# Optimization experiments

Hardware: AMD Instinct MI355X
Metric: run time of the kernel (lower is better)

## Reference

```python
import jax, jax.numpy as jnp
import numpy as np

N, E = 50000, 800000
D, H = 256, 256
OA, OS, OE = 21, 2, 5


def _sage(x, src, dst, wl, bl, wr):
    # PyG SAGEConv: out = lin_l(mean_{j in N(i)} x_j) + lin_r(x_i); bias lives in lin_l
    n = x.shape[0]
    msg = x[src]                                            # [E, d] gather
    agg = jax.ops.segment_sum(msg, dst, num_segments=n)     # [N, d]
    cnt = jax.ops.segment_sum(jnp.ones((src.shape[0],), x.dtype), dst, num_segments=n)
    mean = agg / jnp.maximum(cnt, 1.0)[:, None]
    return mean @ wl.T + bl + x @ wr.T


def _bn(x, g, b, eps=1e-5):
    mu = x.mean(axis=0)
    var = x.var(axis=0)
    return (x - mu) * jax.lax.rsqrt(var + eps) * g + b


def setup_inputs() -> dict:
    key = jax.random.key(0)
    ks = jax.random.split(key, 32)

    def lin(k, o, i):
        s = 1.0 / np.sqrt(i)
        k1, k2 = jax.random.split(k)
        return (jax.random.uniform(k1, (o, i), jnp.float32, -s, s),
                jax.random.uniform(k2, (o,), jnp.float32, -s, s))

    w1l, b1 = lin(ks[3], H, D); w1r, _ = lin(ks[4], H, D)
    w2l, b2 = lin(ks[5], H, H); w2r, _ = lin(ks[6], H, H)
    w3l, b3 = lin(ks[7], H, H); w3r, _ = lin(ks[8], H, H)
    wal, ba = lin(ks[9], OA, H); war, _ = lin(ks[10], OA, H)
    wsl, bs = lin(ks[11], OS, H); wsr, _ = lin(ks[12], OS, H)
    wel, be = lin(ks[13], OE, H); wer, _ = lin(ks[14], OE, H)

    return {
        'x': jax.random.normal(ks[0], (N, D), jnp.float32),
        'edge_src': jax.random.randint(ks[1], (E,), 0, N),
        'edge_dst': jax.random.randint(ks[2], (E,), 0, N),
        'w1l': w1l, 'b1': b1, 'w1r': w1r, 'g1': jnp.ones((H,), jnp.float32), 'bt1': jnp.zeros((H,), jnp.float32),
        'w2l': w2l, 'b2': b2, 'w2r': w2r, 'g2': jnp.ones((H,), jnp.float32), 'bt2': jnp.zeros((H,), jnp.float32),
        'w3l': w3l, 'b3': b3, 'w3r': w3r, 'g3': jnp.ones((H,), jnp.float32), 'bt3': jnp.zeros((H,), jnp.float32),
        'wal': wal, 'ba': ba, 'war': war,
        'wsl': wsl, 'bs': bs, 'wsr': wsr,
        'wel': wel, 'be': be, 'wer': wer,
    }


def reference(x, edge_src, edge_dst,
              w1l, b1, w1r, g1, bt1,
              w2l, b2, w2r, g2, bt2,
              w3l, b3, w3r, g3, bt3,
              wal, ba, war, wsl, bs, wsr, wel, be, wer):
    h = jax.nn.relu(_bn(_sage(x, edge_src, edge_dst, w1l, b1, w1r), g1, bt1))
    h = jax.nn.relu(_bn(_sage(h, edge_src, edge_dst, w2l, b2, w2r), g2, bt2))
    h = jax.nn.relu(_bn(_sage(h, edge_src, edge_dst, w3l, b3, w3r), g3, bt3))
    # dropout is identity in eval mode
    age = _sage(h, edge_src, edge_dst, wal, ba, war)
    sex = _sage(h, edge_src, edge_dst, wsl, bs, wsr)
    eth = _sage(h, edge_src, edge_dst, wel, be, wer)
    return age, sex, eth
```

## Files before the change

kernel.cpp:

```cpp
#include <hip/hip_runtime.h>
#include <hip/hip_bf16.h>
#include <cstddef>

#define HD 256
#define KD 512
#define NH 28

typedef __attribute__((ext_vector_type(8))) short bf16x8;
typedef __attribute__((ext_vector_type(4))) float f32x4;

__device__ inline float bf2f(unsigned short u) { return __uint_as_float(((unsigned)u) << 16); }
__device__ inline unsigned short f2bf(float f) {
    __hip_bfloat16 h = __float2bfloat16(f);
    return *(unsigned short*)&h;
}

__global__ void hist_kernel(const int* __restrict__ dst, int* __restrict__ cnt, int E) {
    int e = blockIdx.x * blockDim.x + threadIdx.x;
    if (e < E) atomicAdd(&cnt[dst[e]], 1);
}

__global__ void chunk_reduce_kernel(const int* __restrict__ cnt, int* __restrict__ bsum, int n) {
    __shared__ int sdata[4];
    int idx = blockIdx.x * 256 + threadIdx.x;
    int v = (idx < n) ? cnt[idx] : 0;
    for (int off = 32; off > 0; off >>= 1) v += __shfl_down(v, off, 64);
    int lane = threadIdx.x & 63, wv = threadIdx.x >> 6;
    if (lane == 0) sdata[wv] = v;
    __syncthreads();
    if (threadIdx.x == 0) bsum[blockIdx.x] = sdata[0] + sdata[1] + sdata[2] + sdata[3];
}

__global__ void scan_chunks_kernel(const int* __restrict__ bsum, int* __restrict__ boff,
                                   int nchunks, int* __restrict__ row_ptr_end, int E) {
    int t = threadIdx.x;
    int v = (t < nchunks) ? bsum[t] : 0;
    int lane = t & 63, wv = t >> 6;
    int incl = v;
    for (int off = 1; off < 64; off <<= 1) { int u = __shfl_up(incl, off, 64); if (lane >= off) incl += u; }
    __shared__ int wsum[4];
    if (lane == 63) wsum[wv] = incl;
    __syncthreads();
    int base = 0;
    for (int w2 = 0; w2 < 4; ++w2) if (w2 < wv) base += wsum[w2];
    if (t < nchunks) boff[t] = base + incl - v;
    if (t == 0) *row_ptr_end = E;
}

__global__ void scan_final_kernel(const int* __restrict__ cnt, const int* __restrict__ boff,
                                  int* __restrict__ row_ptr, float* __restrict__ invdeg, int n) {
    int idx = blockIdx.x * 256 + threadIdx.x;
    int v = (idx < n) ? cnt[idx] : 0;
    int lane = threadIdx.x & 63, wv = threadIdx.x >> 6;
    int incl = v;
    for (int off = 1; off < 64; off <<= 1) { int u = __shfl_up(incl, off, 64); if (lane >= off) incl += u; }
    __shared__ int wsum[4];
    if (lane == 63) wsum[wv] = incl;
    __syncthreads();
    int base = 0;
    for (int w2 = 0; w2 < 4; ++w2) if (w2 < wv) base += wsum[w2];
    if (idx < n) {
        row_ptr[idx] = boff[blockIdx.x] + base + incl - v;
        invdeg[idx] = 1.0f / fmaxf((float)v, 1.0f);
    }
}

__global__ void scatter_kernel(const int* __restrict__ src, const int* __restrict__ dst,
                               const int* __restrict__ row_ptr, int* __restrict__ cursor,
                               int* __restrict__ col_idx, int E) {
    int e = blockIdx.x * blockDim.x + threadIdx.x;
    if (e < E) {
        int d = dst[e];
        int pos = atomicAdd(&cursor[d], 1);
        col_idx[row_ptr[d] + pos] = src[e];
    }
}

__global__ void pack_layer_w(const float* __restrict__ wl, const float* __restrict__ wr,
                             unsigned short* __restrict__ dst) {
    int idx = blockIdx.x * 256 + threadIdx.x;
    if (idx >= HD * KD) return;
    int nn = idx >> 9, k = idx & 511;
    float v = (k < HD) ? wl[nn * HD + k] : wr[nn * HD + (k - HD)];
    dst[idx] = f2bf(v);
}

__global__ void pack_heads2(const float* __restrict__ wal, const float* __restrict__ war,
                            const float* __restrict__ wsl, const float* __restrict__ wsr,
                            const float* __restrict__ wel, const float* __restrict__ wer,
                            const float* __restrict__ ba, const float* __restrict__ bs,
                            const float* __restrict__ be,
                            unsigned short* __restrict__ W2, float* __restrict__ bcat) {
    int idx = blockIdx.x * 256 + threadIdx.x;
    if (idx >= 64 * HD) return;
    int o = idx >> 8, k = idx & 255;
    float v = 0.f;
    if (o < 21)                    v = wal[o * HD + k];
    else if (o < 23)               v = wsl[(o - 21) * HD + k];
    else if (o < 28)               v = wel[(o - 23) * HD + k];
    else if (o >= 32 && o < 53)    v = war[(o - 32) * HD + k];
    else if (o >= 53 && o < 55)    v = wsr[(o - 53) * HD + k];
    else if (o >= 55 && o < 60)    v = wer[(o - 55) * HD + k];
    W2[idx] = f2bf(v);
    if (k == 0 && o < 32) {
        float b = 0.f;
        if (o < 21) b = ba[o]; else if (o < 23) b = bs[o - 21]; else if (o < 28) b = be[o - 23];
        bcat[o] = b;
    }
}

__global__ void convert_x_kernel(const float* __restrict__ x, unsigned short* __restrict__ buf, int n) {
    int idx = blockIdx.x * 256 + threadIdx.x;
    if (idx >= n * 64) return;
    int r = idx >> 6, c4 = (idx & 63) * 4;
    float4 v = ((const float4*)x)[idx];
    ushort4 o;
    o.x = f2bf(v.x); o.y = f2bf(v.y); o.z = f2bf(v.z); o.w = f2bf(v.w);
    *(ushort4*)&buf[(size_t)r * KD + HD + c4] = o;
}

__global__ void agg_mean_bf16(unsigned short* __restrict__ buf,
                              const int* __restrict__ row_ptr, const int* __restrict__ col_idx,
                              const float* __restrict__ invdeg, int n) {
    int half = threadIdx.x >> 5;
    int l32 = threadIdx.x & 31;
    int node = blockIdx.x * 8 + half;
    if (node >= n) return;
    int s = row_ptr[node], e = row_ptr[node + 1];
    int coff = HD + l32 * 8;
    float a[8];
#pragma unroll
    for (int k = 0; k < 8; ++k) a[k] = 0.f;
    int i = s;
    for (; i + 4 <= e; i += 4) {
        int s0 = col_idx[i], s1 = col_idx[i + 1], s2 = col_idx[i + 2], s3 = col_idx[i + 3];
        float4 v0 = *(const float4*)&buf[(size_t)s0 * KD + coff];
        float4 v1 = *(const float4*)&buf[(size_t)s1 * KD + coff];
        float4 v2 = *(const float4*)&buf[(size_t)s2 * KD + coff];
        float4 v3 = *(const float4*)&buf[(size_t)s3 * KD + coff];
        const unsigned short* u0 = (const unsigned short*)&v0;
        const unsigned short* u1 = (const unsigned short*)&v1;
        const unsigned short* u2 = (const unsigned short*)&v2;
        const unsigned short* u3 = (const unsigned short*)&v3;
#pragma unroll
        for (int k = 0; k < 8; ++k) a[k] += bf2f(u0[k]) + bf2f(u1[k]) + bf2f(u2[k]) + bf2f(u3[k]);
    }
    for (; i < e; ++i) {
        int s0 = col_idx[i];
        float4 v = *(const float4*)&buf[(size_t)s0 * KD + coff];
        const unsigned short* u = (const unsigned short*)&v;
#pragma unroll
        for (int k = 0; k < 8; ++k) a[k] += bf2f(u[k]);
    }
    float inv = invdeg[node];
    ushort4 o0, o1;
    o0.x = f2bf(a[0] * inv); o0.y = f2bf(a[1] * inv); o0.z = f2bf(a[2] * inv); o0.w = f2bf(a[3] * inv);
    o1.x = f2bf(a[4] * inv); o1.y = f2bf(a[5] * inv); o1.z = f2bf(a[6] * inv); o1.w = f2bf(a[7] * inv);
    *(ushort4*)&buf[(size_t)node * KD + l32 * 8] = o0;
    *(ushort4*)&buf[(size_t)node * KD + l32 * 8 + 4] = o1;
}

#define SWIZ(row, kc) (((row) << 6) + ((((kc) ^ ((row) & 7))) << 3))

__global__ __launch_bounds__(512) void gemm_mfma_stats(
        const unsigned short* __restrict__ A, const unsigned short* __restrict__ W,
        unsigned short* __restrict__ Zb,
        float* __restrict__ colsum, float* __restrict__ colsumsq, int n) {
    __shared__ __align__(16) short As[128 * 64];
    __shared__ __align__(16) short Bs[256 * 64];
    int t = threadIdx.x;
    int wave = t >> 6, lane = t & 63;
    int wm = wave & 1, wn = wave >> 1;
    int lm = lane & 15, q = lane >> 4;
    int r0 = blockIdx.x * 128;

    f32x4 acc[4][4];
#pragma unroll
    for (int i = 0; i < 4; ++i)
#pragma unroll
        for (int j = 0; j < 4; ++j) acc[i][j] = (f32x4){0.f, 0.f, 0.f, 0.f};

    int srow = t >> 3;
    int skc = t & 7;

    for (int kt = 0; kt < 8; ++kt) {
        int kc = kt * 64;
#pragma unroll
        for (int u = 0; u < 2; ++u) {
            int row = srow + u * 64;
            int ga = r0 + row; if (ga >= n) ga = n - 1;
            *(float4*)&As[SWIZ(row, skc)] = *(const float4*)&A[(size_t)ga * KD + kc + skc * 8];
        }
#pragma unroll
        for (int u = 0; u < 4; ++u) {
            int row = srow + u * 64;
            *(float4*)&Bs[SWIZ(row, skc)] = *(const float4*)&W[(size_t)row * KD + kc + skc * 8];
        }
        __syncthreads();
#pragma unroll
        for (int kk = 0; kk < 2; ++kk) {
            bf16x8 af[4], bfv[4];
#pragma unroll
            for (int i = 0; i < 4; ++i)
                af[i] = *(bf16x8*)&As[SWIZ(wm * 64 + i * 16 + lm, kk * 4 + q)];
#pragma unroll
            for (int j = 0; j < 4; ++j)
                bfv[j] = *(bf16x8*)&Bs[SWIZ(wn * 64 + j * 16 + lm, kk * 4 + q)];
#pragma unroll
            for (int i = 0; i < 4; ++i)
#pragma unroll
                for (int j = 0; j < 4; ++j)
                    acc[i][j] = __builtin_amdgcn_mfma_f32_16x16x32_bf16(af[i], bfv[j], acc[i][j], 0, 0, 0);
        }
        __syncthreads();
    }

    float s[4], s2[4];
#pragma unroll
    for (int j = 0; j < 4; ++j) { s[j] = 0.f; s2[j] = 0.f; }
#pragma unroll
    for (int i = 0; i < 4; ++i) {
        int rbase = r0 + wm * 64 + i * 16 + q * 4;
#pragma unroll
        for (int reg = 0; reg < 4; ++reg) {
            int r = rbase + reg;
            if (r < n) {
#pragma unroll
                for (int j = 0; j < 4; ++j) {
                    float v = acc[i][j][reg];
                    int c = wn * 64 + j * 16 + lm;
                    Zb[(size_t)r * KD + HD + c] = f2bf(v);
                    s[j] += v; s2[j] += v * v;
                }
            }
        }
    }
#pragma unroll
    for (int j = 0; j < 4; ++j) {
        s[j]  += __shfl_xor(s[j], 16, 64);  s[j]  += __shfl_xor(s[j], 32, 64);
        s2[j] += __shfl_xor(s2[j], 16, 64); s2[j] += __shfl_xor(s2[j], 32, 64);
    }
    if (lane < 16) {
#pragma unroll
        for (int j = 0; j < 4; ++j) {
            int c = wn * 64 + j * 16 + lm;
            atomicAdd(&colsum[c], s[j]);
            atomicAdd(&colsumsq[c], s2[j]);
        }
    }
}

__global__ void bn_finalize_kernel(const float* __restrict__ colsum, const float* __restrict__ colsumsq,
                                   const float* __restrict__ g, const float* __restrict__ bt,
                                   float* __restrict__ scale, float* __restrict__ shift, int n) {
    int c = threadIdx.x;
    float fn = (float)n;
    float mu = colsum[c] / fn;
    float var = colsumsq[c] / fn - mu * mu;
    float sc = g[c] / sqrtf(var + 1e-5f);
    scale[c] = sc;
    shift[c] = bt[c] - mu * sc;
}

__global__ void bn_apply_relu_kernel(unsigned short* __restrict__ buf, const float* __restrict__ scale,
                                     const float* __restrict__ shift, int total4) {
    int idx = blockIdx.x * blockDim.x + threadIdx.x;
    if (idx >= total4) return;
    int r = idx >> 6, c4 = (idx & 63) * 4;
    unsigned short* p = &buf[(size_t)r * KD + HD + c4];
    ushort4 z = *(ushort4*)p;
    float4 sc = *(const float4*)&scale[c4];
    float4 sh = *(const float4*)&shift[c4];
    ushort4 o;
    o.x = f2bf(fmaxf(bf2f(z.x) * sc.x + sh.x, 0.f));
    o.y = f2bf(fmaxf(bf2f(z.y) * sc.y + sh.y, 0.f));
    o.z = f2bf(fmaxf(bf2f(z.z) * sc.z + sh.z, 0.f));
    o.w = f2bf(fmaxf(bf2f(z.w) * sc.w + sh.w, 0.f));
    *(ushort4*)p = o;
}

__global__ __launch_bounds__(256) void heads_pgemm(const unsigned short* __restrict__ A,
                                                   const unsigned short* __restrict__ W2,
                                                   unsigned short* __restrict__ PL,
                                                   unsigned short* __restrict__ PR, int n) {
    __shared__ __align__(16) short As[128 * 64];
    __shared__ __align__(16) short Bs[64 * 64];
    int t = threadIdx.x;
    int wave = t >> 6, lane = t & 63;
    int lm = lane & 15, q = lane >> 4;
    int r0 = blockIdx.x * 128;

    f32x4 acc[2][4];
#pragma unroll
    for (int i = 0; i < 2; ++i)
#pragma unroll
        for (int j = 0; j < 4; ++j) acc[i][j] = (f32x4){0.f, 0.f, 0.f, 0.f};

    int srow = t >> 3;
    int skc = t & 7;

    for (int kt = 0; kt < 4; ++kt) {
        int kc = kt * 64;
#pragma unroll
        for (int u = 0; u < 4; ++u) {
            int row = srow + u * 32;
            int ga = r0 + row; if (ga >= n) ga = n - 1;
            *(float4*)&As[SWIZ(row, skc)] = *(const float4*)&A[(size_t)ga * KD + kc + skc * 8];
        }
#pragma unroll
        for (int u = 0; u < 2; ++u) {
            int c = t + u * 256;
            int row = c >> 3, kcc = c & 7;
            *(float4*)&Bs[SWIZ(row, kcc)] = *(const float4*)&W2[(size_t)row * HD + kc + kcc * 8];
        }
        __syncthreads();
#pragma unroll
        for (int kk = 0; kk < 2; ++kk) {
            bf16x8 af[2], bfv[4];
#pragma unroll
            for (int i = 0; i < 2; ++i)
                af[i] = *(bf16x8*)&As[SWIZ(wave * 32 + i * 16 + lm, kk * 4 + q)];
#pragma unroll
            for (int j = 0; j < 4; ++j)
                bfv[j] = *(bf16x8*)&Bs[SWIZ(j * 16 + lm, kk * 4 + q)];
#pragma unroll
            for (int i = 0; i < 2; ++i)
#pragma unroll
                for (int j = 0; j < 4; ++j)
                    acc[i][j] = __builtin_amdgcn_mfma_f32_16x16x32_bf16(af[i], bfv[j], acc[i][j], 0, 0, 0);
        }
        __syncthreads();
    }
#pragma unroll
    for (int i = 0; i < 2; ++i) {
        int rbase = r0 + wave * 32 + i * 16 + q * 4;
#pragma unroll
        for (int reg = 0; reg < 4; ++reg) {
            int r = rbase + reg;
            if (r >= n) continue;
#pragma unroll
            for (int j = 0; j < 4; ++j) {
                int c = j * 16 + lm;
                unsigned short v = f2bf(acc[i][j][reg]);
                if (c < 32) PL[(size_t)r * 32 + c] = v;
                else        PR[(size_t)r * 32 + (c - 32)] = v;
            }
        }
    }
}

__global__ void head_agg(const unsigned short* __restrict__ PL, const unsigned short* __restrict__ PR,
                         const int* __restrict__ row_ptr, const int* __restrict__ col_idx,
                         const float* __restrict__ invdeg, const float* __restrict__ bcat,
                         float* __restrict__ out, int n) {
    int t = threadIdx.x;
    int sub = t >> 4;
    int l16 = t & 15;
    int node = blockIdx.x * 16 + sub;
    if (node >= n) return;
    int s = row_ptr[node], e = row_ptr[node + 1];
    int off = l16 * 2;
    float a0 = 0.f, a1 = 0.f;
    int i = s;
    for (; i + 4 <= e; i += 4) {
        int s0 = col_idx[i], s1 = col_idx[i + 1], s2 = col_idx[i + 2], s3 = col_idx[i + 3];
        unsigned v0 = *(const unsigned*)&PL[(size_t)s0 * 32 + off];
        unsigned v1 = *(const unsigned*)&PL[(size_t)s1 * 32 + off];
        unsigned v2 = *(const unsigned*)&PL[(size_t)s2 * 32 + off];
        unsigned v3 = *(const unsigned*)&PL[(size_t)s3 * 32 + off];
        a0 += bf2f((unsigned short)v0) + bf2f((unsigned short)v1) + bf2f((unsigned short)v2) + bf2f((unsigned short)v3);
        a1 += bf2f((unsigned short)(v0 >> 16)) + bf2f((unsigned short)(v1 >> 16))
            + bf2f((unsigned short)(v2 >> 16)) + bf2f((unsigned short)(v3 >> 16));
    }
    for (; i < e; ++i) {
        unsigned v = *(const unsigned*)&PL[(size_t)col_idx[i] * 32 + off];
        a0 += bf2f((unsigned short)v);
        a1 += bf2f((unsigned short)(v >> 16));
    }
    float inv = invdeg[node];
    unsigned vr = *(const unsigned*)&PR[(size_t)node * 32 + off];
    float o0 = a0 * inv + bf2f((unsigned short)vr) + bcat[off];
    float o1 = a1 * inv + bf2f((unsigned short)(vr >> 16)) + bcat[off + 1];
    int c0 = off, c1 = off + 1;
    if (c0 < 21)      out[(size_t)node * 21 + c0] = o0;
    else if (c0 < 23) out[(size_t)n * 21 + (size_t)node * 2 + (c0 - 21)] = o0;
    else if (c0 < 28) out[(size_t)n * 23 + (size_t)node * 5 + (c0 - 23)] = o0;
    if (c1 < 21)      out[(size_t)node * 21 + c1] = o1;
    else if (c1 < 23) out[(size_t)n * 21 + (size_t)node * 2 + (c1 - 21)] = o1;
    else if (c1 < 28) out[(size_t)n * 23 + (size_t)node * 5 + (c1 - 23)] = o1;
}

static inline char* align256(char* p) {
    return (char*)(((uintptr_t)p + 255) & ~(uintptr_t)255);
}

extern "C" void kernel_launch(void* const* d_in, const int* in_sizes, int n_in,
                              void* d_out, int out_size, void* d_ws, size_t ws_size,
                              hipStream_t stream) {
    const float* x    = (const float*)d_in[0];
    const int*   esrc = (const int*)d_in[1];
    const int*   edst = (const int*)d_in[2];
    const float* w1l = (const float*)d_in[3];  const float* w1r = (const float*)d_in[5];
    const float* g1  = (const float*)d_in[6];  const float* bt1 = (const float*)d_in[7];
    const float* w2l = (const float*)d_in[8];  const float* w2r = (const float*)d_in[10];
    const float* g2  = (const float*)d_in[11]; const float* bt2 = (const float*)d_in[12];
    const float* w3l = (const float*)d_in[13]; const float* w3r = (const float*)d_in[15];
    const float* g3  = (const float*)d_in[16]; const float* bt3 = (const float*)d_in[17];
    const float* wal = (const float*)d_in[18]; const float* ba = (const float*)d_in[19];
    const float* war = (const float*)d_in[20];
    const float* wsl = (const float*)d_in[21]; const float* bs = (const float*)d_in[22];
    const float* wsr = (const float*)d_in[23];
    const float* wel = (const float*)d_in[24]; const float* be = (const float*)d_in[25];
    const float* wer = (const float*)d_in[26];
    float* out = (float*)d_out;

    int N = in_sizes[0] / HD;
    int E = in_sizes[1];

    char* p = (char*)d_ws;
    size_t HB = (size_t)N * KD * sizeof(unsigned short);
    unsigned short* buf0 = (unsigned short*)p; p += HB;
    unsigned short* buf1 = (unsigned short*)p; p += HB;
    p = align256(p);
    unsigned short* PLb = (unsigned short*)p; p += (size_t)N * 32 * sizeof(unsigned short);
    unsigned short* PRb = (unsigned short*)p; p += (size_t)N * 32 * sizeof(unsigned short);
    p = align256(p);
    int* col_idx = (int*)p; p += sizeof(int) * (size_t)E;       p = align256(p);
    int* row_ptr = (int*)p; p += sizeof(int) * (size_t)(N + 1); p = align256(p);
    int* cnt     = (int*)p; p += sizeof(int) * (size_t)N;
    int* cursor  = (int*)p; p += sizeof(int) * (size_t)N;       p = align256(p);
    int* bsum    = (int*)p; p += sizeof(int) * 256;
    int* boff    = (int*)p; p += sizeof(int) * 256;             p = align256(p);
    float* invdeg   = (float*)p; p += sizeof(float) * (size_t)N; p = align256(p);
    float* colsum   = (float*)p; p += sizeof(float) * 256;
    float* colsumsq = (float*)p; p += sizeof(float) * 256;       p = align256(p);
    float* scale    = (float*)p; p += sizeof(float) * 256;
    float* shift    = (float*)p; p += sizeof(float) * 256;       p = align256(p);
    unsigned short* wc1 = (unsigned short*)p; p += sizeof(unsigned short) * HD * KD;
    unsigned short* wc2 = (unsigned short*)p; p += sizeof(unsigned short) * HD * KD;
    unsigned short* wc3 = (unsigned short*)p; p += sizeof(unsigned short) * HD * KD;
    unsigned short* w2h = (unsigned short*)p; p += sizeof(unsigned short) * 64 * HD;
    p = align256(p);
    float* bcat = (float*)p; p += sizeof(float) * 32;
    (void)ws_size; (void)n_in; (void)out_size;

    int nchunks = (N + 255) / 256;

    hipMemsetAsync(cnt, 0, sizeof(int) * 2 * (size_t)N, stream);
    hist_kernel<<<(E + 255) / 256, 256, 0, stream>>>(edst, cnt, E);
    chunk_reduce_kernel<<<nchunks, 256, 0, stream>>>(cnt, bsum, N);
    scan_chunks_kernel<<<1, 256, 0, stream>>>(bsum, boff, nchunks, &row_ptr[N], E);
    scan_final_kernel<<<nchunks, 256, 0, stream>>>(cnt, boff, row_ptr, invdeg, N);
    scatter_kernel<<<(E + 255) / 256, 256, 0, stream>>>(esrc, edst, row_ptr, cursor, col_idx, E);
    pack_layer_w<<<(HD * KD + 255) / 256, 256, 0, stream>>>(w1l, w1r, wc1);
    pack_layer_w<<<(HD * KD + 255) / 256, 256, 0, stream>>>(w2l, w2r, wc2);
    pack_layer_w<<<(HD * KD + 255) / 256, 256, 0, stream>>>(w3l, w3r, wc3);
    pack_heads2<<<(64 * HD + 255) / 256, 256, 0, stream>>>(wal, war, wsl, wsr, wel, wer,
                                                           ba, bs, be, w2h, bcat);
    convert_x_kernel<<<(N * 64 + 255) / 256, 256, 0, stream>>>(x, buf0, N);

    int aggGrid = (N + 7) / 8;
    int gemmGrid = (N + 127) / 128;
    int total4 = N * 64;

    unsigned short* cur = buf0;
    unsigned short* nxt = buf1;
    const unsigned short* wcs[3] = {wc1, wc2, wc3};
    const float* gs[3]  = {g1, g2, g3};
    const float* bts[3] = {bt1, bt2, bt3};

    for (int l = 0; l < 3; ++l) {
        agg_mean_bf16<<<aggGrid, 256, 0, stream>>>(cur, row_ptr, col_idx, invdeg, N);
        hipMemsetAsync(colsum, 0, sizeof(float) * 512, stream);
        gemm_mfma_stats<<<gemmGrid, 512, 0, stream>>>(cur, wcs[l], nxt, colsum, colsumsq, N);
        bn_finalize_kernel<<<1, 256, 0, stream>>>(colsum, colsumsq, gs[l], bts[l], scale, shift, N);
        bn_apply_relu_kernel<<<(total4 + 255) / 256, 256, 0, stream>>>(nxt, scale, shift, total4);
        unsigned short* t2 = cur; cur = nxt; nxt = t2;
    }

    heads_pgemm<<<gemmGrid, 256, 0, stream>>>(cur + HD, w2h, PLb, PRb, N);
    head_agg<<<(N + 15) / 16, 256, 0, stream>>>(PLb, PRb, row_ptr, col_idx, invdeg, bcat, out, N);
}
```

Before: 571.4 us.

## Fuse BatchNorm finalize and ReLU into downstream aggregation and GEMM loads

```diff
diff --git a/kernel.cpp b/kernel.cpp
--- a/kernel.cpp
+++ b/kernel.cpp
@@ -1,6 +1,7 @@
 #include <hip/hip_runtime.h>
 #include <hip/hip_bf16.h>
 #include <cstddef>
+#include <cfloat>
 
 #define HD 256
 #define KD 512
@@ -119,45 +120,85 @@
     *(ushort4*)&buf[(size_t)r * KD + HD + c4] = o;
 }
 
-__global__ void agg_mean_bf16(unsigned short* __restrict__ buf,
-                              const int* __restrict__ row_ptr, const int* __restrict__ col_idx,
-                              const float* __restrict__ invdeg, int n) {
-    int half = threadIdx.x >> 5;
-    int l32 = threadIdx.x & 31;
-    int node = blockIdx.x * 8 + half;
+__global__ __launch_bounds__(256) void agg_mean_fused(
+        unsigned short* __restrict__ buf,
+        const int* __restrict__ row_ptr, const int* __restrict__ col_idx,
+        const float* __restrict__ invdeg,
+        const float* __restrict__ psum, const float* __restrict__ psumsq,
+        const float* __restrict__ g, const float* __restrict__ bt,
+        float* __restrict__ zsum, float* __restrict__ zsumsq,
+        int apply, int n) {
+    __shared__ float sc_s[HD], sh_s[HD];
+    int t = threadIdx.x;
+    if (blockIdx.x == 0) { zsum[t] = 0.f; zsumsq[t] = 0.f; }
+    if (apply) {
+        float fn = (float)n;
+        float mu = psum[t] / fn;
+        float var = psumsq[t] / fn - mu * mu;
+        float s = g[t] / sqrtf(var + 1e-5f);
+        sc_s[t] = s; sh_s[t] = bt[t] - mu * s;
+    } else { sc_s[t] = 1.f; sh_s[t] = 0.f; }
+    __syncthreads();
+
+    int wv = t >> 6, lane = t & 63;
+    int node = blockIdx.x * 4 + wv;
     if (node >= n) return;
+    int par = lane >> 5;
+    int c16 = lane & 31;
+    float lo = apply ? 0.f : -FLT_MAX;
+    float sc_r[8], sh_r[8];
+#pragma unroll
+    for (int k = 0; k < 8; ++k) { sc_r[k] = sc_s[c16 * 8 + k]; sh_r[k] = sh_s[c16 * 8 + k]; }
+    const unsigned short* src = buf + HD + c16 * 8;
     int s = row_ptr[node], e = row_ptr[node + 1];
-    int coff = HD + l32 * 8;
     float a[8];
 #pragma unroll
     for (int k = 0; k < 8; ++k) a[k] = 0.f;
     int i = s;
-    for (; i + 4 <= e; i += 4) {
-        int s0 = col_idx[i], s1 = col_idx[i + 1], s2 = col_idx[i + 2], s3 = col_idx[i + 3];
-        float4 v0 = *(const float4*)&buf[(size_t)s0 * KD + coff];
-        float4 v1 = *(const float4*)&buf[(size_t)s1 * KD + coff];
-        float4 v2 = *(const float4*)&buf[(size_t)s2 * KD + coff];
-        float4 v3 = *(const float4*)&buf[(size_t)s3 * KD + coff];
+    for (; i + 8 <= e; i += 8) {
+        int j0 = col_idx[i + par];
+        int j1 = col_idx[i + 2 + par];
+        int j2 = col_idx[i + 4 + par];
+        int j3 = col_idx[i + 6 + par];
+        float4 v0 = *(const float4*)(src + (size_t)j0 * KD);
+        float4 v1 = *(const float4*)(src + (size_t)j1 * KD);
+        float4 v2 = *(const float4*)(src + (size_t)j2 * KD);
+        float4 v3 = *(const float4*)(src + (size_t)j3 * KD);
         const unsigned short* u0 = (const unsigned short*)&v0;
         const unsigned short* u1 = (const unsigned short*)&v1;
         const unsigned short* u2 = (const unsigned short*)&v2;
         const unsigned short* u3 = (const unsigned short*)&v3;
 #pragma unroll
-        for (int k = 0; k < 8; ++k) a[k] += bf2f(u0[k]) + bf2f(u1[k]) + bf2f(u2[k]) + bf2f(u3[k]);
-    }
-    for (; i < e; ++i) {
-        int s0 = col_idx[i];
-        float4 v = *(const float4*)&buf[(size_t)s0 * KD + coff];
+        for (int k = 0; k < 8; ++k) {
+            a[k] += fmaxf(bf2f(u0[k]) * sc_r[k] + sh_r[k], lo);
+            a[k] += fmaxf(bf2f(u1[k]) * sc_r[k] + sh_r[k], lo);
+            a[k] += fmaxf(bf2f(u2[k]) * sc_r[k] + sh_r[k], lo);
+            a[k] += fmaxf(bf2f(u3[k]) * sc_r[k] + sh_r[k], lo);
+        }
+    }
+    for (; i + 2 <= e; i += 2) {
+        int j = col_idx[i + par];
+        float4 v = *(const float4*)(src + (size_t)j * KD);
         const unsigned short* u = (const unsigned short*)&v;
 #pragma unroll
-        for (int k = 0; k < 8; ++k) a[k] += bf2f(u[k]);
-    }
+        for (int k = 0; k < 8; ++k) a[k] += fmaxf(bf2f(u[k]) * sc_r[k] + sh_r[k], lo);
+    }
+    if (i < e) {
+        int j = col_idx[i];
+        float4 v = *(const float4*)(src + (size_t)j * KD);
+        const unsigned short* u = (const unsigned short*)&v;
+        if (par == 0) {
+#pragma unroll
+            for (int k = 0; k < 8; ++k) a[k] += fmaxf(bf2f(u[k]) * sc_r[k] + sh_r[k], lo);
+        }
+    }
+#pragma unroll
+    for (int k = 0; k < 8; ++k) a[k] += __shfl_xor(a[k], 32, 64);
     float inv = invdeg[node];
-    ushort4 o0, o1;
-    o0.x = f2bf(a[0] * inv); o0.y = f2bf(a[1] * inv); o0.z = f2bf(a[2] * inv); o0.w = f2bf(a[3] * inv);
-    o1.x = f2bf(a[4] * inv); o1.y = f2bf(a[5] * inv); o1.z = f2bf(a[6] * inv); o1.w = f2bf(a[7] * inv);
-    *(ushort4*)&buf[(size_t)node * KD + l32 * 8] = o0;
-    *(ushort4*)&buf[(size_t)node * KD + l32 * 8 + 4] = o1;
+    unsigned short ob[8];
+#pragma unroll
+    for (int k = 0; k < 8; ++k) ob[k] = f2bf(a[k] * inv);
+    if (par == 0) *(float4*)&buf[(size_t)node * KD + c16 * 8] = *(const float4*)ob;
 }
 
 #define SWIZ(row, kc) (((row) << 6) + ((((kc) ^ ((row) & 7))) << 3))
@@ -165,10 +206,26 @@
 __global__ __launch_bounds__(512) void gemm_mfma_stats(
         const unsigned short* __restrict__ A, const unsigned short* __restrict__ W,
         unsigned short* __restrict__ Zb,
-        float* __restrict__ colsum, float* __restrict__ colsumsq, int n) {
+        const float* __restrict__ psum, const float* __restrict__ psumsq,
+        const float* __restrict__ g, const float* __restrict__ bt,
+        float* __restrict__ colsum, float* __restrict__ colsumsq,
+        int apply, int n) {
     __shared__ __align__(16) short As[128 * 64];
     __shared__ __align__(16) short Bs[256 * 64];
+    __shared__ float sc_s[HD], sh_s[HD];
     int t = threadIdx.x;
+    if (t < HD) {
+        if (apply) {
+            float fn = (float)n;
+            float mu = psum[t] / fn;
+            float var = psumsq[t] / fn - mu * mu;
+            float s = g[t] / sqrtf(var + 1e-5f);
+            sc_s[t] = s; sh_s[t] = bt[t] - mu * s;
+        } else { sc_s[t] = 1.f; sh_s[t] = 0.f; }
+    }
+    __syncthreads();
+    float lo = apply ? 0.f : -FLT_MAX;
+
     int wave = t >> 6, lane = t & 63;
     int wm = wave & 1, wn = wave >> 1;
     int lm = lane & 15, q = lane >> 4;
@@ -185,11 +242,27 @@
 
     for (int kt = 0; kt < 8; ++kt) {
         int kc = kt * 64;
+        bool rh = (kt >= 4);
+        float scr[8], shr[8];
+        if (rh) {
+            int cb = kc - HD + skc * 8;
+            *(float4*)&scr[0] = *(const float4*)&sc_s[cb];
+            *(float4*)&scr[4] = *(const float4*)&sc_s[cb + 4];
+            *(float4*)&shr[0] = *(const float4*)&sh_s[cb];
+            *(float4*)&shr[4] = *(const float4*)&sh_s[cb + 4];
+        }
 #pragma unroll
         for (int u = 0; u < 2; ++u) {
             int row = srow + u * 64;
             int ga = r0 + row; if (ga >= n) ga = n - 1;
-            *(float4*)&As[SWIZ(row, skc)] = *(const float4*)&A[(size_t)ga * KD + kc + skc * 8];
+            float4 av = *(const float4*)&A[(size_t)ga * KD + kc + skc * 8];
+            if (rh) {
+                unsigned short* us = (unsigned short*)&av;
+#pragma unroll
+                for (int k2 = 0; k2 < 8; ++k2)
+                    us[k2] = f2bf(fmaxf(bf2f(us[k2]) * scr[k2] + shr[k2], lo));
+            }
+            *(float4*)&As[SWIZ(row, skc)] = av;
         }
 #pragma unroll
         for (int u = 0; u < 4; ++u) {
@@ -250,42 +323,27 @@
     }
 }
 
-__global__ void bn_finalize_kernel(const float* __restrict__ colsum, const float* __restrict__ colsumsq,
-                                   const float* __restrict__ g, const float* __restrict__ bt,
-                                   float* __restrict__ scale, float* __restrict__ shift, int n) {
-    int c = threadIdx.x;
-    float fn = (float)n;
-    float mu = colsum[c] / fn;
-    float var = colsumsq[c] / fn - mu * mu;
-    float sc = g[c] / sqrtf(var + 1e-5f);
-    scale[c] = sc;
-    shift[c] = bt[c] - mu * sc;
-}
-
-__global__ void bn_apply_relu_kernel(unsigned short* __restrict__ buf, const float* __restrict__ scale,
-                                     const float* __restrict__ shift, int total4) {
-    int idx = blockIdx.x * blockDim.x + threadIdx.x;
-    if (idx >= total4) return;
-    int r = idx >> 6, c4 = (idx & 63) * 4;
-    unsigned short* p = &buf[(size_t)r * KD + HD + c4];
-    ushort4 z = *(ushort4*)p;
-    float4 sc = *(const float4*)&scale[c4];
-    float4 sh = *(const float4*)&shift[c4];
-    ushort4 o;
-    o.x = f2bf(fmaxf(bf2f(z.x) * sc.x + sh.x, 0.f));
-    o.y = f2bf(fmaxf(bf2f(z.y) * sc.y + sh.y, 0.f));
-    o.z = f2bf(fmaxf(bf2f(z.z) * sc.z + sh.z, 0.f));
-    o.w = f2bf(fmaxf(bf2f(z.w) * sc.w + sh.w, 0.f));
-    *(ushort4*)p = o;
-}
-
 __global__ __launch_bounds__(256) void heads_pgemm(const unsigned short* __restrict__ A,
                                                    const unsigned short* __restrict__ W2,
+                                                   const float* __restrict__ psum,
+                                                   const float* __restrict__ psumsq,
+                                                   const float* __restrict__ g,
+                                                   const float* __restrict__ bt,
                                                    unsigned short* __restrict__ PL,
                                                    unsigned short* __restrict__ PR, int n) {
     __shared__ __align__(16) short As[128 * 64];
     __shared__ __align__(16) short Bs[64 * 64];
+    __shared__ float sc_s[HD], sh_s[HD];
     int t = threadIdx.x;
+    {
+        float fn = (float)n;
+        float mu = psum[t] / fn;
+        float var = psumsq[t] / fn - mu * mu;
+        float s = g[t] / sqrtf(var + 1e-5f);
+        sc_s[t] = s; sh_s[t] = bt[t] - mu * s;
+    }
+    __syncthreads();
+
     int wave = t >> 6, lane = t & 63;
     int lm = lane & 15, q = lane >> 4;
     int r0 = blockIdx.x * 128;
@@ -301,11 +359,24 @@
 
     for (int kt = 0; kt < 4; ++kt) {
         int kc = kt * 64;
+        float scr[8], shr[8];
+        {
+            int cb = kc + skc * 8;
+            *(float4*)&scr[0] = *(const float4*)&sc_s[cb];
+            *(float4*)&scr[4] = *(const float4*)&sc_s[cb + 4];
+            *(float4*)&shr[0] = *(const float4*)&sh_s[cb];
+            *(float4*)&shr[4] = *(const float4*)&sh_s[cb + 4];
+        }
 #pragma unroll
         for (int u = 0; u < 4; ++u) {
             int row = srow + u * 32;
             int ga = r0 + row; if (ga >= n) ga = n - 1;
-            *(float4*)&As[SWIZ(row, skc)] = *(const float4*)&A[(size_t)ga * KD + kc + skc * 8];
+            float4 av = *(const float4*)&A[(size_t)ga * KD + kc + skc * 8];
+            unsigned short* us = (unsigned short*)&av;
+#pragma unroll
+            for (int k2 = 0; k2 < 8; ++k2)
+                us[k2] = f2bf(fmaxf(bf2f(us[k2]) * scr[k2] + shr[k2], 0.f));
+            *(float4*)&As[SWIZ(row, skc)] = av;
         }
 #pragma unroll
         for (int u = 0; u < 2; ++u) {
@@ -432,10 +503,12 @@
     int* bsum    = (int*)p; p += sizeof(int) * 256;
     int* boff    = (int*)p; p += sizeof(int) * 256;             p = align256(p);
     float* invdeg   = (float*)p; p += sizeof(float) * (size_t)N; p = align256(p);
-    float* colsum   = (float*)p; p += sizeof(float) * 256;
-    float* colsumsq = (float*)p; p += sizeof(float) * 256;       p = align256(p);
-    float* scale    = (float*)p; p += sizeof(float) * 256;
-    float* shift    = (float*)p; p += sizeof(float) * 256;       p = align256(p);
+    float* zs[3]; float* zq[3];
+    for (int l = 0; l < 3; ++l) {
+        zs[l] = (float*)p; p += sizeof(float) * 256;
+        zq[l] = (float*)p; p += sizeof(float) * 256;
+    }
+    p = align256(p);
     unsigned short* wc1 = (unsigned short*)p; p += sizeof(unsigned short) * HD * KD;
     unsigned short* wc2 = (unsigned short*)p; p += sizeof(unsigned short) * HD * KD;
     unsigned short* wc3 = (unsigned short*)p; p += sizeof(unsigned short) * HD * KD;
@@ -459,9 +532,8 @@
                                                            ba, bs, be, w2h, bcat);
     convert_x_kernel<<<(N * 64 + 255) / 256, 256, 0, stream>>>(x, buf0, N);
 
-    int aggGrid = (N + 7) / 8;
+    int aggGrid = (N + 3) / 4;
     int gemmGrid = (N + 127) / 128;
-    int total4 = N * 64;
 
     unsigned short* cur = buf0;
     unsigned short* nxt = buf1;
@@ -470,14 +542,18 @@
     const float* bts[3] = {bt1, bt2, bt3};
 
     for (int l = 0; l < 3; ++l) {
-        agg_mean_bf16<<<aggGrid, 256, 0, stream>>>(cur, row_ptr, col_idx, invdeg, N);
-        hipMemsetAsync(colsum, 0, sizeof(float) * 512, stream);
-        gemm_mfma_stats<<<gemmGrid, 512, 0, stream>>>(cur, wcs[l], nxt, colsum, colsumsq, N);
-        bn_finalize_kernel<<<1, 256, 0, stream>>>(colsum, colsumsq, gs[l], bts[l], scale, shift, N);
-        bn_apply_relu_kernel<<<(total4 + 255) / 256, 256, 0, stream>>>(nxt, scale, shift, total4);
+        const float* ps = (l > 0) ? zs[l - 1] : zs[0];
+        const float* pq = (l > 0) ? zq[l - 1] : zq[0];
+        const float* pg = (l > 0) ? gs[l - 1] : g1;
+        const float* pb = (l > 0) ? bts[l - 1] : bt1;
+        int apply = (l > 0) ? 1 : 0;
+        agg_mean_fused<<<aggGrid, 256, 0, stream>>>(cur, row_ptr, col_idx, invdeg,
+                                                    ps, pq, pg, pb, zs[l], zq[l], apply, N);
+        gemm_mfma_stats<<<gemmGrid, 512, 0, stream>>>(cur, wcs[l], nxt,
+                                                      ps, pq, pg, pb, zs[l], zq[l], apply, N);
         unsigned short* t2 = cur; cur = nxt; nxt = t2;
     }
 
-    heads_pgemm<<<gemmGrid, 256, 0, stream>>>(cur + HD, w2h, PLb, PRb, N);
+    heads_pgemm<<<gemmGrid, 256, 0, stream>>>(cur + HD, w2h, zs[2], zq[2], g3, bt3, PLb, PRb, N);
     head_agg<<<(N + 15) / 16, 256, 0, stream>>>(PLb, PRb, row_ptr, col_idx, invdeg, bcat, out, N);
 }
```

Result: no change. 582.9 us (+2.0%).
